# Performance work log

Measured on AMD Instinct MI355X. Metric: run time of the kernel, lower is better.

## Reference

```python
import jax, jax.numpy as jnp
import numpy as np

B, K, D, H, T, S = 8192, 32, 768, 256, 16, 2  # batch, candidates, d_model, hidden, topics, shots
MAX_SHOT = 8
TEMP = 0.1


def _l2n(x, eps=1e-12):
    return x / jnp.clip(jnp.linalg.norm(x, axis=-1, keepdims=True), eps)


def setup_inputs() -> dict:
    key = jax.random.key(0)
    ks = jax.random.split(key, 20)
    f32 = jnp.float32
    rn = lambda k, shape, s: jax.random.normal(k, shape, f32) * s
    inp = {}
    inp['query_emb'] = jax.random.normal(ks[0], (B, D), f32)
    inp['cand_emb'] = jax.random.normal(ks[1], (B, K, D), f32)
    inp['W_in'] = rn(ks[2], (H, D), 0.03)              # input_proj (bias=False)
    inp['Wq_a'] = rn(ks[3], (H, H), 0.05)              # MHA in-proj q
    inp['Wk_a'] = rn(ks[4], (H, H), 0.05)
    inp['Wv_a'] = rn(ks[5], (H, H), 0.05)
    inp['bq_a'] = jnp.zeros((H,), f32)
    inp['bk_a'] = jnp.zeros((H,), f32)
    inp['bv_a'] = jnp.zeros((H,), f32)
    inp['Wo_a'] = rn(ks[6], (H, H), 0.05)              # MHA out-proj
    inp['bo_a'] = jnp.zeros((H,), f32)
    inp['ln_w'] = jnp.ones((H,), f32)
    inp['ln_b'] = jnp.zeros((H,), f32)
    inp['Wq'] = jnp.eye(H, dtype=f32) + rn(ks[7], (H, H), 0.01)   # query_proj (eye init + noise)
    inp['Wc'] = jnp.eye(H, dtype=f32) + rn(ks[8], (H, H), 0.01)   # cand_proj
    inp['W_ih'] = rn(ks[9], (3 * H, H), 0.05)          # GRUCell ih (r,z,n)
    inp['W_hh'] = rn(ks[10], (3 * H, H), 0.05)
    inp['b_ih'] = jnp.zeros((3 * H,), f32)
    inp['b_hh'] = jnp.zeros((3 * H,), f32)
    inp['step_emb'] = rn(ks[11], (MAX_SHOT, H), 0.02)
    inp['topic_protos'] = rn(ks[12], (T, H), 0.02)
    inp['Wqt'] = rn(ks[13], (T, H), 0.05)              # query_topic_head
    inp['bqt'] = jnp.zeros((T,), f32)
    inp['cover_lambda'] = jnp.array(-2.0, f32)
    return inp


def reference(query_emb, cand_emb, W_in, Wq_a, Wk_a, Wv_a, bq_a, bk_a, bv_a,
              Wo_a, bo_a, ln_w, ln_b, Wq, Wc, W_ih, W_hh, b_ih, b_hh,
              step_emb, topic_protos, Wqt, bqt, cover_lambda):
    Bd = query_emb.shape[0]
    # input projection 768 -> 256
    qr = query_emb @ W_in.T                                # [B,H]
    cr = jnp.einsum('bkd,hd->bkh', cand_emb, W_in)         # [B,K,H]
    # single-head cross-attention (query len 1, eval mode -> no dropout)
    q = qr @ Wq_a.T + bq_a
    k = jnp.einsum('bkh,gh->bkg', cr, Wk_a) + bk_a
    v = jnp.einsum('bkh,gh->bkg', cr, Wv_a) + bv_a
    attn = jax.nn.softmax(jnp.einsum('bh,bkh->bk', q, k) / jnp.sqrt(jnp.float32(H)))
    ctx = jnp.einsum('bk,bkh->bh', attn, v) @ Wo_a.T + bo_a
    # residual + LayerNorm
    x = ctx + qr
    mu = jnp.mean(x, -1, keepdims=True)
    var = jnp.var(x, -1, keepdims=True)
    qe = (x - mu) / jnp.sqrt(var + 1e-5) * ln_w + ln_b
    # pointer projections + L2 normalize
    h = _l2n(qe @ Wq.T)                                    # [B,H]
    cn = _l2n(jnp.einsum('bkh,gh->bkg', cr, Wc))           # [B,K,H]
    topic_probs = jax.nn.softmax(jnp.einsum('bkh,th->bkt', cn, _l2n(topic_protos)))  # [B,K,T]
    need = jax.nn.softmax(h @ Wqt.T + bqt)                 # [B,T]
    lam = jax.nn.softplus(cover_lambda)
    sel = jnp.zeros((Bd, K), bool)
    covered = jnp.zeros((Bd, T), jnp.float32)
    rows = jnp.arange(Bd)
    logits, preds = [], []
    for step in range(S):
        h_step = _l2n(h + step_emb[min(step, MAX_SHOT - 1)])
        scores = jnp.einsum('bh,bkh->bk', h_step, cn) / TEMP
        if step > 0:
            uncov = jnp.clip(1.0 - covered, 0.0, 1.0)
            gain = jnp.einsum('bt,bkt->bk', need * uncov, topic_probs)
            scores = scores + lam * gain
        scores = jnp.where(sel, -100.0, scores)
        logits.append(scores)
        idx = jnp.argmax(scores, axis=-1)                  # labels=None -> greedy feedback
        preds.append(idx)
        sel = sel.at[rows, idx].set(True)
        chosen = cn[rows, idx]                             # [B,H]
        covered = jnp.minimum(covered + topic_probs[rows, idx], 1.0)
        # GRUCell update
        gi = chosen @ W_ih.T + b_ih
        gh = h @ W_hh.T + b_hh
        ir, iz, ig = jnp.split(gi, 3, axis=-1)
        hr, hz, hg = jnp.split(gh, 3, axis=-1)
        r = jax.nn.sigmoid(ir + hr)
        z = jax.nn.sigmoid(iz + hz)
        n = jnp.tanh(ig + r * hg)
        h = _l2n((1.0 - z) * n + z * h)
    return jnp.stack(logits, 1), jnp.stack(preds, 1)       # [B,S,K], [B,S]
```

## Files before the change

kernel.cpp:

```cpp
#include <hip/hip_runtime.h>
#include <math.h>

#define B_ 8192
#define K_ 32
#define D_ 768
#define H_ 256
#define T_ 16
#define S_ 2

typedef unsigned int uint;
typedef unsigned short ushort;
typedef __attribute__((ext_vector_type(8))) short bf16x8;
typedef __attribute__((ext_vector_type(4))) float f32x4;

__device__ __forceinline__ float wsum(float v) {
  v += __shfl_xor(v, 32); v += __shfl_xor(v, 16); v += __shfl_xor(v, 8);
  v += __shfl_xor(v, 4);  v += __shfl_xor(v, 2);  v += __shfl_xor(v, 1);
  return v;
}
__device__ __forceinline__ float wmaxr(float v) {
  v = fmaxf(v, __shfl_xor(v, 32)); v = fmaxf(v, __shfl_xor(v, 16));
  v = fmaxf(v, __shfl_xor(v, 8));  v = fmaxf(v, __shfl_xor(v, 4));
  v = fmaxf(v, __shfl_xor(v, 2));  v = fmaxf(v, __shfl_xor(v, 1));
  return v;
}

__device__ __forceinline__ void split4(const float4 f, uint2& h, uint2& lo) {
  const uint ux = __float_as_uint(f.x), uy = __float_as_uint(f.y);
  const uint uz = __float_as_uint(f.z), uw = __float_as_uint(f.w);
  h.x = (uy & 0xFFFF0000u) | (ux >> 16);
  h.y = (uw & 0xFFFF0000u) | (uz >> 16);
  const float rx = f.x - __uint_as_float(ux & 0xFFFF0000u);
  const float ry = f.y - __uint_as_float(uy & 0xFFFF0000u);
  const float rz = f.z - __uint_as_float(uz & 0xFFFF0000u);
  const float rw = f.w - __uint_as_float(uw & 0xFFFF0000u);
  lo.x = (__float_as_uint(ry) & 0xFFFF0000u) | (__float_as_uint(rx) >> 16);
  lo.y = (__float_as_uint(rw) & 0xFFFF0000u) | (__float_as_uint(rz) >> 16);
}


__global__ __launch_bounds__(256)
void fold_kernel(const float* __restrict__ Wk_a, const float* __restrict__ Wv_a,
                 const float* __restrict__ Wc,  const float* __restrict__ W_in,
                 float* __restrict__ WkinT, float* __restrict__ Wv_in,
                 ushort* __restrict__ Bh, ushort* __restrict__ Bl)
{
  const int i = blockIdx.x;
  const int m = blockIdx.y;
  const float* Wx = (m == 0) ? Wk_a : ((m == 1) ? Wv_a : Wc);
  const int t = threadIdx.x;
  float a0 = 0.f, a1 = 0.f, a2 = 0.f;
  for (int k = 0; k < H_; k++) {
    const float wv = Wx[i * H_ + k];
    const float* row = W_in + (size_t)k * D_;
    a0 = fmaf(wv, row[t], a0);
    a1 = fmaf(wv, row[t + 256], a1);
    a2 = fmaf(wv, row[t + 512], a2);
  }
  if (m == 0) {
    WkinT[(size_t)t * H_ + i] = a0;
    WkinT[(size_t)(t + 256) * H_ + i] = a1;
    WkinT[(size_t)(t + 512) * H_ + i] = a2;
  } else if (m == 1) {
    float* o = Wv_in + (size_t)i * D_;
    o[t] = a0; o[t + 256] = a1; o[t + 512] = a2;
  } else {
    const float vals[3] = {a0, a1, a2};
#pragma unroll
    for (int j = 0; j < 3; j++) {
      const int k = t + j * 256;
      const float v = vals[j];
      const int idx = (((k >> 5) * 16 + (i >> 4)) * 64 + ((i & 15) | (((k >> 3) & 3) << 4))) * 8 + (k & 7);
      const uint u = __float_as_uint(v);
      Bh[idx] = (ushort)(u >> 16);
      const float rr = v - __uint_as_float(u & 0xFFFF0000u);
      Bl[idx] = (ushort)(__float_as_uint(rr) >> 16);
    }
  }
}

__global__ __launch_bounds__(256)
void tile_kernel(const float* __restrict__ W, int NB, int K,
                 ushort* __restrict__ Bh, ushort* __restrict__ Bl)
{
  const int n = blockIdx.x, t = threadIdx.x;
  for (int k = t; k < K; k += 256) {
    const float v = W[(size_t)n * K + k];
    const int idx = (((k >> 5) * NB + (n >> 4)) * 64 + ((n & 15) | (((k >> 3) & 3) << 4))) * 8 + (k & 7);
    const uint u = __float_as_uint(v);
    Bh[idx] = (ushort)(u >> 16);
    const float rr = v - __uint_as_float(u & 0xFFFF0000u);
    Bl[idx] = (ushort)(__float_as_uint(rr) >> 16);
  }
}

__global__ __launch_bounds__(256)
void proto_kernel(const float* __restrict__ tpro, float* __restrict__ pro)
{
  const int w = threadIdx.x >> 6, l = threadIdx.x & 63;
  for (int r = w; r < T_; r += 4) {
    const float4 v = *(const float4*)(tpro + (size_t)r * H_ + l * 4);
    const float n = fmaxf(sqrtf(wsum(v.x * v.x + v.y * v.y + v.z * v.z + v.w * v.w)), 1e-12f);
    float4 o; o.x = v.x / n; o.y = v.y / n; o.z = v.z / n; o.w = v.w / n;
    *(float4*)(pro + (size_t)r * H_ + l * 4) = o;
  }
}

__global__ __launch_bounds__(256)
void fold2_kernel(const float* __restrict__ Wq_a, const float* __restrict__ bq_a,
                  const float* __restrict__ bk_a, const float* __restrict__ Wo_a,
                  const float* __restrict__ bo_a, const float* __restrict__ bv_a,
                  const float* __restrict__ Wq,   const float* __restrict__ ln_w,
                  const float* __restrict__ ln_b, const float* __restrict__ WkinT,
                  const float* __restrict__ Wv_in,
                  float* __restrict__ Bqk, float* __restrict__ bqk,
                  float* __restrict__ Wvo, float* __restrict__ bvo,
                  float* __restrict__ Wqp, float* __restrict__ bqp,
                  float* __restrict__ vqbk, float* __restrict__ qcst)
{
  __shared__ float rd_s[4];
  const int n = blockIdx.x, t = threadIdx.x, w = t >> 6, l = t & 63;
  float s = 0.f;
  for (int hh = 0; hh < H_; hh++)
    s = fmaf(Wq_a[hh * H_ + t], WkinT[(size_t)n * H_ + hh], s);
  Bqk[(size_t)n * H_ + t] = s;
  float p = bq_a[t] * WkinT[(size_t)n * H_ + t];
  p = wsum(p);
  if (l == 0) rd_s[w] = p;
  __syncthreads();
  if (t == 0) bqk[n] = rd_s[0] + rd_s[1] + rd_s[2] + rd_s[3];
  if (n < H_) {
    float a0 = 0.f, a1 = 0.f, a2 = 0.f;
    for (int hh = 0; hh < H_; hh++) {
      const float wo = Wo_a[n * H_ + hh];
      const float* rowv = Wv_in + (size_t)hh * D_;
      a0 = fmaf(wo, rowv[t], a0);
      a1 = fmaf(wo, rowv[t + 256], a1);
      a2 = fmaf(wo, rowv[t + 512], a2);
    }
    Wvo[(size_t)n * D_ + t] = a0;
    Wvo[(size_t)n * D_ + t + 256] = a1;
    Wvo[(size_t)n * D_ + t + 512] = a2;
    float pb = Wo_a[n * H_ + t] * bv_a[t];
    pb = wsum(pb);
    __syncthreads();
    if (l == 0) rd_s[w] = pb;
    __syncthreads();
    if (t == 0) bvo[n] = rd_s[0] + rd_s[1] + rd_s[2] + rd_s[3] + bo_a[n];
    Wqp[n * H_ + t] = Wq[n * H_ + t] * ln_w[t];
    float pq = Wq[n * H_ + t] * ln_b[t];
    pq = wsum(pq);
    __syncthreads();
    if (l == 0) rd_s[w] = pq;
    __syncthreads();
    if (t == 0) bqp[n] = rd_s[0] + rd_s[1] + rd_s[2] + rd_s[3];
  }
  if (n == 0) {
    float sv = 0.f;
    for (int hh = 0; hh < H_; hh++) sv = fmaf(bk_a[hh], Wq_a[hh * H_ + t], sv);
    vqbk[t] = sv;
    float pc = bq_a[t] * bk_a[t];
    pc = wsum(pc);
    __syncthreads();
    if (l == 0) rd_s[w] = pc;
    __syncthreads();
    if (t == 0) qcst[0] = rd_s[0] + rd_s[1] + rd_s[2] + rd_s[3];
  }
}

__global__ __launch_bounds__(256)
void gemm_cn(const float* __restrict__ A, const ushort* __restrict__ Bh,
             const ushort* __restrict__ Bl, float* __restrict__ C)
{
  __shared__ __align__(16) ushort AhS[2][2048], AlS[2][2048];
  __shared__ float rsq[64][4];
  const int t = threadIdx.x, l = t & 63, w = t >> 6;
  const int r = t >> 2, kc = t & 3;
  const float* Ag = A + ((size_t)blockIdx.x * 64 + r) * 768 + kc * 8;
  const int aslot = ((r >> 4) * 64 + ((r & 15) | (kc << 4))) * 8;
  const ushort* Bhb = Bh + ((w * 4) * 64 + l) * 8;
  const ushort* Blb = Bl + ((w * 4) * 64 + l) * 8;

  f32x4 acc[4][4];
#pragma unroll
  for (int i = 0; i < 4; i++)
#pragma unroll
    for (int j = 0; j < 4; j++) acc[i][j] = (f32x4)0.f;

  float4 f0 = *(const float4*)(Ag);
  float4 f1 = *(const float4*)(Ag + 4);
  {
    uint2 ha, la, hb, lb;
    split4(f0, ha, la); split4(f1, hb, lb);
    *(uint4*)&AhS[0][aslot] = make_uint4(ha.x, ha.y, hb.x, hb.y);
    *(uint4*)&AlS[0][aslot] = make_uint4(la.x, la.y, lb.x, lb.y);
  }
  f0 = *(const float4*)(Ag + 32);
  f1 = *(const float4*)(Ag + 36);
  __syncthreads();

#pragma unroll 2
  for (int ks = 0; ks < 24; ks++) {
    const int cur = ks & 1;
    uint4 bhv[4], blv[4];
#pragma unroll
    for (int ni = 0; ni < 4; ni++) {
      bhv[ni] = *(const uint4*)(Bhb + ks * 8192 + ni * 512);
      blv[ni] = *(const uint4*)(Blb + ks * 8192 + ni * 512);
    }
    if (ks < 23) {
      uint2 ha, la, hb, lb;
      split4(f0, ha, la); split4(f1, hb, lb);
      *(uint4*)&AhS[cur ^ 1][aslot] = make_uint4(ha.x, ha.y, hb.x, hb.y);
      *(uint4*)&AlS[cur ^ 1][aslot] = make_uint4(la.x, la.y, lb.x, lb.y);
      if (ks < 22) {
        f0 = *(const float4*)(Ag + (ks + 2) * 32);
        f1 = *(const float4*)(Ag + (ks + 2) * 32 + 4);
      }
    }
#pragma unroll
    for (int mi = 0; mi < 4; mi++) {
      const bf16x8 ah = *(const bf16x8*)&AhS[cur][(mi * 64 + l) * 8];
      const bf16x8 al = *(const bf16x8*)&AlS[cur][(mi * 64 + l) * 8];
#pragma unroll
      for (int ni = 0; ni < 4; ni++) {
        const bf16x8 bhf = *(const bf16x8*)&bhv[ni];
        const bf16x8 blf = *(const bf16x8*)&blv[ni];
        acc[mi][ni] = __builtin_amdgcn_mfma_f32_16x16x32_bf16(ah, bhf, acc[mi][ni], 0, 0, 0);
        acc[mi][ni] = __builtin_amdgcn_mfma_f32_16x16x32_bf16(al, bhf, acc[mi][ni], 0, 0, 0);
        acc[mi][ni] = __builtin_amdgcn_mfma_f32_16x16x32_bf16(ah, blf, acc[mi][ni], 0, 0, 0);
      }
    }
    __syncthreads();
  }

#pragma unroll
  for (int mi = 0; mi < 4; mi++)
#pragma unroll
    for (int rg = 0; rg < 4; rg++) {
      float p = 0.f;
#pragma unroll
      for (int ni = 0; ni < 4; ni++) { const float v = acc[mi][ni][rg]; p = fmaf(v, v, p); }
      p += __shfl_xor(p, 1); p += __shfl_xor(p, 2); p += __shfl_xor(p, 4); p += __shfl_xor(p, 8);
      if ((l & 15) == 0) rsq[mi * 16 + (l >> 4) * 4 + rg][w] = p;
    }
  __syncthreads();
  const size_t row0 = (size_t)blockIdx.x * 64;
#pragma unroll
  for (int mi = 0; mi < 4; mi++)
#pragma unroll
    for (int rg = 0; rg < 4; rg++) {
      const int rl = mi * 16 + (l >> 4) * 4 + rg;
      const float ssum = rsq[rl][0] + rsq[rl][1] + rsq[rl][2] + rsq[rl][3];
      const float inv = 1.f / fmaxf(sqrtf(ssum), 1e-12f);
#pragma unroll
      for (int ni = 0; ni < 4; ni++)
        C[(row0 + rl) * H_ + w * 64 + ni * 16 + (l & 15)] = acc[mi][ni][rg] * inv;
    }
}

__global__ __launch_bounds__(256)
void tp_kernel(const float* __restrict__ cn, const float* __restrict__ pro,
               float* __restrict__ tp)
{
  __shared__ float cn_s[16][260];
  __shared__ float pro_s[16][260];
  const int t = threadIdx.x;
  const size_t row0 = (size_t)blockIdx.x * 16;
  const int sr = t >> 4;
#pragma unroll
  for (int j = 0; j < 4; j++) {
    const int c = (t & 15) * 4 + j * 64;
    *(float4*)&cn_s[sr][c] = *(const float4*)(cn + (row0 + sr) * H_ + c);
    *(float4*)&pro_s[sr][c] = *(const float4*)(pro + sr * H_ + c);
  }
  __syncthreads();
  const int r = t >> 4, tt = t & 15;
  float d = 0.f;
#pragma unroll 8
  for (int j = 0; j < 64; j++) {
    const float4 a = *(const float4*)&cn_s[r][j * 4];
    const float4 p = *(const float4*)&pro_s[tt][j * 4];
    d = fmaf(a.x, p.x, d); d = fmaf(a.y, p.y, d);
    d = fmaf(a.z, p.z, d); d = fmaf(a.w, p.w, d);
  }
  float m = d;
  m = fmaxf(m, __shfl_xor(m, 1)); m = fmaxf(m, __shfl_xor(m, 2));
  m = fmaxf(m, __shfl_xor(m, 4)); m = fmaxf(m, __shfl_xor(m, 8));
  const float e = expf(d - m);
  float su = e;
  su += __shfl_xor(su, 1); su += __shfl_xor(su, 2);
  su += __shfl_xor(su, 4); su += __shfl_xor(su, 8);
  tp[(row0 + r) * T_ + tt] = e / su;
}

template<int NKS, int NB, bool BIAS>
__global__ __launch_bounds__(256)
void gemm_bf(const float* __restrict__ A, const ushort* __restrict__ Bh,
             const ushort* __restrict__ Bl, const float* __restrict__ bias,
             float* __restrict__ C)
{
  __shared__ __align__(16) ushort AhS[2][4096], AlS[2][4096];
  const int t = threadIdx.x, l = t & 63, w = t >> 6;
  const int wr = w >> 1, wc = w & 1;
  const int Kd = NKS * 32, N = NB * 16;
  const int r = t >> 1, kc0 = (t & 1) * 2;
  const float* Ag = A + ((size_t)blockIdx.x * 128 + r) * Kd + kc0 * 8;
  const int aslot0 = ((r >> 4) * 64 + ((r & 15) | (kc0 << 4))) * 8;
  const int aslot1 = aslot0 + 128;
  const int nb0 = blockIdx.y * 4 + wc * 2;
  const ushort* Bhb = Bh + (nb0 * 64 + l) * 8;
  const ushort* Blb = Bl + (nb0 * 64 + l) * 8;

  f32x4 acc[4][2];
#pragma unroll
  for (int i = 0; i < 4; i++)
#pragma unroll
    for (int j = 0; j < 2; j++) acc[i][j] = (f32x4)0.f;

  float4 f0 = *(const float4*)(Ag);
  float4 f1 = *(const float4*)(Ag + 4);
  float4 f2 = *(const float4*)(Ag + 8);
  float4 f3 = *(const float4*)(Ag + 12);
  {
    uint2 ha, la, hb, lb;
    split4(f0, ha, la); split4(f1, hb, lb);
    *(uint4*)&AhS[0][aslot0] = make_uint4(ha.x, ha.y, hb.x, hb.y);
    *(uint4*)&AlS[0][aslot0] = make_uint4(la.x, la.y, lb.x, lb.y);
    split4(f2, ha, la); split4(f3, hb, lb);
    *(uint4*)&AhS[0][aslot1] = make_uint4(ha.x, ha.y, hb.x, hb.y);
    *(uint4*)&AlS[0][aslot1] = make_uint4(la.x, la.y, lb.x, lb.y);
  }
  f0 = *(const float4*)(Ag + 32); f1 = *(const float4*)(Ag + 36);
  f2 = *(const float4*)(Ag + 40); f3 = *(const float4*)(Ag + 44);
  __syncthreads();

#pragma unroll 2
  for (int ks = 0; ks < NKS; ks++) {
    const int cur = ks & 1;
    uint4 bhv[2], blv[2];
#pragma unroll
    for (int ni = 0; ni < 2; ni++) {
      bhv[ni] = *(const uint4*)(Bhb + ks * (NB * 512) + ni * 512);
      blv[ni] = *(const uint4*)(Blb + ks * (NB * 512) + ni * 512);
    }
    if (ks < NKS - 1) {
      uint2 ha, la, hb, lb;
      split4(f0, ha, la); split4(f1, hb, lb);
      *(uint4*)&AhS[cur ^ 1][aslot0] = make_uint4(ha.x, ha.y, hb.x, hb.y);
      *(uint4*)&AlS[cur ^ 1][aslot0] = make_uint4(la.x, la.y, lb.x, lb.y);
      split4(f2, ha, la); split4(f3, hb, lb);
      *(uint4*)&AhS[cur ^ 1][aslot1] = make_uint4(ha.x, ha.y, hb.x, hb.y);
      *(uint4*)&AlS[cur ^ 1][aslot1] = make_uint4(la.x, la.y, lb.x, lb.y);
      if (ks < NKS - 2) {
        f0 = *(const float4*)(Ag + (ks + 2) * 32);
        f1 = *(const float4*)(Ag + (ks + 2) * 32 + 4);
        f2 = *(const float4*)(Ag + (ks + 2) * 32 + 8);
        f3 = *(const float4*)(Ag + (ks + 2) * 32 + 12);
      }
    }
#pragma unroll
    for (int mi = 0; mi < 4; mi++) {
      const bf16x8 ah = *(const bf16x8*)&AhS[cur][((wr * 4 + mi) * 64 + l) * 8];
      const bf16x8 al = *(const bf16x8*)&AlS[cur][((wr * 4 + mi) * 64 + l) * 8];
#pragma unroll
      for (int ni = 0; ni < 2; ni++) {
        const bf16x8 bhf = *(const bf16x8*)&bhv[ni];
        const bf16x8 blf = *(const bf16x8*)&blv[ni];
        acc[mi][ni] = __builtin_amdgcn_mfma_f32_16x16x32_bf16(ah, bhf, acc[mi][ni], 0, 0, 0);
        acc[mi][ni] = __builtin_amdgcn_mfma_f32_16x16x32_bf16(al, bhf, acc[mi][ni], 0, 0, 0);
        acc[mi][ni] = __builtin_amdgcn_mfma_f32_16x16x32_bf16(ah, blf, acc[mi][ni], 0, 0, 0);
      }
    }
    __syncthreads();
  }

  const size_t row0 = (size_t)blockIdx.x * 128 + wr * 64;
  const int col0 = blockIdx.y * 64 + wc * 32;
#pragma unroll
  for (int mi = 0; mi < 4; mi++)
#pragma unroll
    for (int ni = 0; ni < 2; ni++) {
      const int col = col0 + ni * 16 + (l & 15);
      const float bb = BIAS ? bias[col] : 0.f;
#pragma unroll
      for (int rg = 0; rg < 4; rg++) {
        const size_t row = row0 + mi * 16 + (l >> 4) * 4 + rg;
        C[row * N + col] = acc[mi][ni][rg] + bb;
      }
    }
}

__global__ __launch_bounds__(256)
void attn_kernel(const float* __restrict__ ce, const float* __restrict__ qkv,
                 const float* __restrict__ qr, const float* __restrict__ vqbk,
                 const float* __restrict__ qcst, float* __restrict__ wce)
{
  __shared__ float4 qk_s[192];
  __shared__ float sc_s[K_];
  __shared__ float at_s[K_];
  __shared__ float rd_s[4];
  const int b = blockIdx.x, t = threadIdx.x;
  const int w = t >> 6, l = t & 63;

  float p = qr[(size_t)b * H_ + t] * vqbk[t];
  p = wsum(p);
  if (l == 0) rd_s[w] = p;
  if (t < 192) qk_s[t] = ((const float4*)qkv)[(size_t)b * 192 + t];
  __syncthreads();
  const float qbk = rd_s[0] + rd_s[1] + rd_s[2] + rd_s[3] + qcst[0];

  const float4* ceb = (const float4*)(ce + (size_t)b * K_ * D_);
#pragma unroll
  for (int cc = 0; cc < 8; cc++) {
    const int c = w * 8 + cc;
    const float4* cr = ceb + c * 192;
    float s = 0.f;
#pragma unroll
    for (int j = 0; j < 3; j++) {
      const float4 f = cr[l + j * 64];
      const float4 q4 = qk_s[l + j * 64];
      s = fmaf(f.x, q4.x, s); s = fmaf(f.y, q4.y, s);
      s = fmaf(f.z, q4.z, s); s = fmaf(f.w, q4.w, s);
    }
    s = wsum(s);
    if (l == 0) sc_s[c] = s + qbk;
  }
  __syncthreads();
  if (w == 0) {
    float s = (l < K_) ? sc_s[l] * (1.f / 16.f) : -1e30f;
    const float m = wmaxr(s);
    float e = (l < K_) ? expf(s - m) : 0.f;
    const float su = wsum(e);
    if (l < K_) at_s[l] = e / su;
  }
  __syncthreads();
  if (t < 192) {
    float4 a = make_float4(0.f, 0.f, 0.f, 0.f);
#pragma unroll
    for (int c = 0; c < K_; c++) {
      const float4 f = ceb[c * 192 + t];
      const float av = at_s[c];
      a.x = fmaf(av, f.x, a.x); a.y = fmaf(av, f.y, a.y);
      a.z = fmaf(av, f.z, a.z); a.w = fmaf(av, f.w, a.w);
    }
    ((float4*)wce)[(size_t)b * 192 + t] = a;
  }
}

__global__ __launch_bounds__(256)
void ln_kernel(const float* __restrict__ xin, const float* __restrict__ res,
               float* __restrict__ xhat)
{
  const int w = threadIdx.x >> 6, l = threadIdx.x & 63;
  const size_t r = (size_t)blockIdx.x * 4 + w;
  const float4 a = *(const float4*)(xin + r * H_ + l * 4);
  const float4 b = *(const float4*)(res + r * H_ + l * 4);
  const float x0 = a.x + b.x, x1 = a.y + b.y, x2 = a.z + b.z, x3 = a.w + b.w;
  const float mu = wsum(x0 + x1 + x2 + x3) * (1.f / H_);
  const float d0 = x0 - mu, d1 = x1 - mu, d2 = x2 - mu, d3 = x3 - mu;
  const float var = wsum(d0 * d0 + d1 * d1 + d2 * d2 + d3 * d3) * (1.f / H_);
  const float isd = 1.f / sqrtf(var + 1e-5f);
  float4 o;
  o.x = d0 * isd; o.y = d1 * isd; o.z = d2 * isd; o.w = d3 * isd;
  *(float4*)(xhat + r * H_ + l * 4) = o;
}

__global__ __launch_bounds__(256)
void h_post(const float* __restrict__ hraw, const float* __restrict__ Wqt,
            const float* __restrict__ bqt, float* __restrict__ h, float* __restrict__ need)
{
  __shared__ float wq_s[T_ * H_];
  for (int i = threadIdx.x; i < T_ * H_; i += 256) wq_s[i] = Wqt[i];
  const int w = threadIdx.x >> 6, l = threadIdx.x & 63;
  const size_t r = (size_t)blockIdx.x * 4 + w;
  const float4 v = *(const float4*)(hraw + r * H_ + l * 4);
  const float n = fmaxf(sqrtf(wsum(v.x * v.x + v.y * v.y + v.z * v.z + v.w * v.w)), 1e-12f);
  float4 hn; hn.x = v.x / n; hn.y = v.y / n; hn.z = v.z / n; hn.w = v.w / n;
  *(float4*)(h + r * H_ + l * 4) = hn;
  __syncthreads();
  float mine = 0.f;
  for (int tt = 0; tt < T_; tt++) {
    const float4 p4 = *(const float4*)(wq_s + tt * H_ + l * 4);
    float p = hn.x * p4.x + hn.y * p4.y + hn.z * p4.z + hn.w * p4.w;
    p = wsum(p);
    if (l == tt) mine = p + bqt[l];
  }
  float s = (l < T_) ? mine : -1e30f;
  const float m = wmaxr(s);
  const float e = (l < T_) ? expf(s - m) : 0.f;
  const float su = wsum(e);
  if (l < T_) need[r * T_ + l] = e / su;
}

template<int STEP>
__global__ __launch_bounds__(256)
void score_kernel(const float* __restrict__ h, const float* __restrict__ se,
                  const float* __restrict__ cn, const float* __restrict__ tp,
                  const float* __restrict__ need, const float* __restrict__ clam,
                  float* __restrict__ covered, int* __restrict__ sel,
                  float* __restrict__ chosen, float* __restrict__ logits,
                  float* __restrict__ preds)
{
  __shared__ __align__(16) float hs_s[H_];
  __shared__ float nu_s[T_];
  __shared__ float sc_s[K_];
  __shared__ float rd_s[4];
  __shared__ int idx_s;
  const int b = blockIdx.x, t = threadIdx.x;
  const int w = t >> 6, l = t & 63;

  const float hv = h[(size_t)b * H_ + t] + se[STEP * H_ + t];
  const float ss = wsum(hv * hv);
  if (l == 0) rd_s[w] = ss;
  if (STEP == 1 && t < T_)
    nu_s[t] = need[(size_t)b * T_ + t] * fminf(fmaxf(1.f - covered[(size_t)b * T_ + t], 0.f), 1.f);
  __syncthreads();
  const float n = fmaxf(sqrtf(rd_s[0] + rd_s[1] + rd_s[2] + rd_s[3]), 1e-12f);
  hs_s[t] = hv / n;
  __syncthreads();

  const float lam = log1pf(expf(clam[0]));
  const float4 hf = *(const float4*)(hs_s + l * 4);
#pragma unroll
  for (int cc = 0; cc < 8; cc++) {
    const int c = w * 8 + cc;
    const float4 cv = *(const float4*)(cn + ((size_t)b * K_ + c) * H_ + l * 4);
    float p = cv.x * hf.x + cv.y * hf.y + cv.z * hf.z + cv.w * hf.w;
    p = wsum(p);
    float s = p / 0.1f;
    if (STEP == 1) {
      float g = (l < T_) ? nu_s[l] * tp[((size_t)b * K_ + c) * T_ + l] : 0.f;
      g = wsum(g);
      s += lam * g;
      if (sel[(size_t)b * K_ + c]) s = -100.f;
    }
    if (l == 0) sc_s[c] = s;
  }
  __syncthreads();
  if (w == 0) {
    float s = (l < K_) ? sc_s[l] : -1e30f;
    int bi = (l < K_) ? l : K_;
#pragma unroll
    for (int o = 32; o; o >>= 1) {
      const float s2 = __shfl_xor(s, o);
      const int i2 = __shfl_xor(bi, o);
      if (s2 > s || (s2 == s && i2 < bi)) { s = s2; bi = i2; }
    }
    if (l == 0) idx_s = bi;
  }
  __syncthreads();
  const int idx = idx_s;
  if (t < K_) logits[(size_t)b * (S_ * K_) + STEP * K_ + t] = sc_s[t];
  if (t == 0) preds[(size_t)b * S_ + STEP] = (float)idx;
  if (STEP == 0) {
    if (t < K_) sel[(size_t)b * K_ + t] = (t == idx) ? 1 : 0;
    if (t < T_) covered[(size_t)b * T_ + t] = fminf(tp[((size_t)b * K_ + idx) * T_ + t], 1.f);
    chosen[(size_t)b * H_ + t] = cn[((size_t)b * K_ + idx) * H_ + t];
  }
}

__global__ __launch_bounds__(256)
void gru_kernel(const float* __restrict__ gi, const float* __restrict__ gh, float* __restrict__ h)
{
  __shared__ float rd_s[4];
  const int b = blockIdx.x, t = threadIdx.x, w = t >> 6, l = t & 63;
  const size_t o = (size_t)b * (3 * H_);
  const float ir = gi[o + t], iz = gi[o + 256 + t], ig = gi[o + 512 + t];
  const float hr = gh[o + t], hz = gh[o + 256 + t], hg = gh[o + 512 + t];
  const float hv = h[(size_t)b * H_ + t];
  const float r = 1.f / (1.f + expf(-(ir + hr)));
  const float z = 1.f / (1.f + expf(-(iz + hz)));
  const float nn = tanhf(ig + r * hg);
  const float x = (1.f - z) * nn + z * hv;
  const float ss = wsum(x * x);
  if (l == 0) rd_s[w] = ss;
  __syncthreads();
  const float n = fmaxf(sqrtf(rd_s[0] + rd_s[1] + rd_s[2] + rd_s[3]), 1e-12f);
  h[(size_t)b * H_ + t] = x / n;
}

extern "C" void kernel_launch(void* const* d_in, const int* in_sizes, int n_in,
                              void* d_out, int out_size, void* d_ws, size_t ws_size,
                              hipStream_t stream)
{
  const float* query_emb = (const float*)d_in[0];
  const float* cand_emb  = (const float*)d_in[1];
  const float* W_in = (const float*)d_in[2];
  const float* Wq_a = (const float*)d_in[3];
  const float* Wk_a = (const float*)d_in[4];
  const float* Wv_a = (const float*)d_in[5];
  const float* bq_a = (const float*)d_in[6];
  const float* bk_a = (const float*)d_in[7];
  const float* bv_a = (const float*)d_in[8];
  const float* Wo_a = (const float*)d_in[9];
  const float* bo_a = (const float*)d_in[10];
  const float* ln_w = (const float*)d_in[11];
  const float* ln_b = (const float*)d_in[12];
  const float* Wq   = (const float*)d_in[13];
  const float* Wc   = (const float*)d_in[14];
  const float* W_ih = (const float*)d_in[15];
  const float* W_hh = (const float*)d_in[16];
  const float* b_ih = (const float*)d_in[17];
  const float* b_hh = (const float*)d_in[18];
  const float* step_emb = (const float*)d_in[19];
  const float* tpro = (const float*)d_in[20];
  const float* Wqt  = (const float*)d_in[21];
  const float* bqt  = (const float*)d_in[22];
  const float* clam = (const float*)d_in[23];

  float* ws = (float*)d_ws;
  size_t o = 0;
  float* WkinT = ws + o; o += (size_t)D_ * H_;
  float* Wv_in = ws + o; o += (size_t)H_ * D_;
  ushort* BhW  = (ushort*)(ws + o); o += 98304;
  ushort* BlW  = (ushort*)(ws + o); o += 98304;
  float* pro   = ws + o; o += (size_t)T_ * H_;
  float* Bqk   = ws + o; o += (size_t)D_ * H_;
  float* bqk   = ws + o; o += 1024;
  float* Wvo   = ws + o; o += (size_t)H_ * D_;
  float* bvo   = ws + o; o += 256;
  float* Wqp   = ws + o; o += (size_t)H_ * H_;
  float* bqp   = ws + o; o += 256;
  float* vqbk  = ws + o; o += 256;
  float* qcst  = ws + o; o += 4;
  ushort* WintH = (ushort*)(ws + o); o += 98304;
  ushort* WintL = (ushort*)(ws + o); o += 98304;
  ushort* BqktH = (ushort*)(ws + o); o += 98304;
  ushort* BqktL = (ushort*)(ws + o); o += 98304;
  ushort* WvotH = (ushort*)(ws + o); o += 98304;
  ushort* WvotL = (ushort*)(ws + o); o += 98304;
  ushort* WqptH = (ushort*)(ws + o); o += 32768;
  ushort* WqptL = (ushort*)(ws + o); o += 32768;
  ushort* WihtH = (ushort*)(ws + o); o += 98304;
  ushort* WihtL = (ushort*)(ws + o); o += 98304;
  ushort* WhhtH = (ushort*)(ws + o); o += 98304;
  ushort* WhhtL = (ushort*)(ws + o); o += 98304;
  float* qr    = ws + o; o += (size_t)B_ * H_;
  float* qkv   = ws + o; o += (size_t)B_ * D_;
  float* wce   = ws + o; o += (size_t)B_ * D_;
  float* ctxb  = ws + o; o += (size_t)B_ * H_;
  float* xhat  = ws + o; o += (size_t)B_ * H_;
  float* h     = ws + o; o += (size_t)B_ * H_;
  float* need  = ws + o; o += (size_t)B_ * T_;
  float* cn    = ws + o; o += (size_t)B_ * K_ * H_;
  float* tp    = ws + o; o += (size_t)B_ * K_ * T_;
  int*   sel   = (int*)(ws + o); o += (size_t)B_ * K_;
  float* cov   = ws + o; o += (size_t)B_ * T_;
  float* chosen= ws + o; o += (size_t)B_ * H_;

  float* out_logits = (float*)d_out;
  float* out_preds  = (float*)d_out + (size_t)B_ * S_ * K_;

  fold_kernel<<<dim3(H_, 3), 256, 0, stream>>>(Wk_a, Wv_a, Wc, W_in, WkinT, Wv_in, BhW, BlW);
  proto_kernel<<<1, 256, 0, stream>>>(tpro, pro);
  fold2_kernel<<<D_, 256, 0, stream>>>(Wq_a, bq_a, bk_a, Wo_a, bo_a, bv_a, Wq, ln_w, ln_b,
                                       WkinT, Wv_in, Bqk, bqk, Wvo, bvo, Wqp, bqp, vqbk, qcst);
  tile_kernel<<<H_, 256, 0, stream>>>(W_in, 16, 768, WintH, WintL);
  tile_kernel<<<D_, 256, 0, stream>>>(Bqk, 48, 256, BqktH, BqktL);
  tile_kernel<<<H_, 256, 0, stream>>>(Wvo, 16, 768, WvotH, WvotL);
  tile_kernel<<<H_, 256, 0, stream>>>(Wqp, 16, 256, WqptH, WqptL);
  tile_kernel<<<D_, 256, 0, stream>>>(W_ih, 48, 256, WihtH, WihtL);
  tile_kernel<<<D_, 256, 0, stream>>>(W_hh, 48, 256, WhhtH, WhhtL);

  gemm_bf<24, 16, false><<<dim3(B_ / 128, 4), 256, 0, stream>>>(query_emb, WintH, WintL, nullptr, qr);
  gemm_bf<8, 48, true><<<dim3(B_ / 128, 12), 256, 0, stream>>>(qr, BqktH, BqktL, bqk, qkv);
  attn_kernel<<<B_, 256, 0, stream>>>(cand_emb, qkv, qr, vqbk, qcst, wce);
  gemm_bf<24, 16, true><<<dim3(B_ / 128, 4), 256, 0, stream>>>(wce, WvotH, WvotL, bvo, ctxb);
  ln_kernel<<<B_ / 4, 256, 0, stream>>>(ctxb, qr, xhat);
  gemm_bf<8, 16, true><<<dim3(B_ / 128, 4), 256, 0, stream>>>(xhat, WqptH, WqptL, bqp, ctxb);
  h_post<<<B_ / 4, 256, 0, stream>>>(ctxb, Wqt, bqt, h, need);

  gemm_cn<<<(B_ * K_) / 64, 256, 0, stream>>>(cand_emb, BhW, BlW, cn);
  tp_kernel<<<(B_ * K_) / 16, 256, 0, stream>>>(cn, pro, tp);

  score_kernel<0><<<B_, 256, 0, stream>>>(h, step_emb, cn, tp, need, clam, cov, sel, chosen, out_logits, out_preds);
  gemm_bf<8, 48, true><<<dim3(B_ / 128, 12), 256, 0, stream>>>(chosen, WihtH, WihtL, b_ih, qkv);
  gemm_bf<8, 48, true><<<dim3(B_ / 128, 12), 256, 0, stream>>>(h, WhhtH, WhhtL, b_hh, wce);
  gru_kernel<<<B_, 256, 0, stream>>>(qkv, wce, h);
  score_kernel<1><<<B_, 256, 0, stream>>>(h, step_emb, cn, tp, need, clam, cov, sel, chosen, out_logits, out_preds);
}
```

Baseline: 1.036 ms.

## Fuse cross-attention into candidate projection GEMM and batch weight tiling launches

The attention-score dot products and the weighted sum over candidate embeddings move into the candidate-projection GEMM, so cand_emb (the largest input) is streamed from DRAM once instead of twice. The six weight-tiling launches are merged into one multi-job kernel. B-fragment loads in both GEMMs are moved next to their MFMA use instead of being prefetched at the top of the k-loop. The fused kernel uses more shared memory and registers and re-reads its candidate tile for the weighted sum, and loading B later may expose global-memory latency.

```diff
diff --git a/kernel.cpp b/kernel.cpp
--- a/kernel.cpp
+++ b/kernel.cpp
@@ -38,6 +38,12 @@
   lo.y = (__float_as_uint(rw) & 0xFFFF0000u) | (__float_as_uint(rz) >> 16);
 }
 
+__device__ __forceinline__ float dot4(const float4 a, const float4 b) {
+  float s = a.x * b.x;
+  s = fmaf(a.y, b.y, s); s = fmaf(a.z, b.z, s); s = fmaf(a.w, b.w, s);
+  return s;
+}
+
 
 __global__ __launch_bounds__(256)
 void fold_kernel(const float* __restrict__ Wk_a, const float* __restrict__ Wv_a,
@@ -79,18 +85,23 @@
   }
 }
 
-__global__ __launch_bounds__(256)
-void tile_kernel(const float* __restrict__ W, int NB, int K,
-                 ushort* __restrict__ Bh, ushort* __restrict__ Bl)
-{
-  const int n = blockIdx.x, t = threadIdx.x;
-  for (int k = t; k < K; k += 256) {
-    const float v = W[(size_t)n * K + k];
-    const int idx = (((k >> 5) * NB + (n >> 4)) * 64 + ((n & 15) | (((k >> 3) & 3) << 4))) * 8 + (k & 7);
+struct TileJob { const float* W; ushort* Bh; ushort* Bl; int NB; int K; int rows; };
+struct TileJobs { TileJob j[6]; };
+
+__global__ __launch_bounds__(256)
+void tile_all(TileJobs jobs)
+{
+  const TileJob J = jobs.j[blockIdx.y];
+  const int n = blockIdx.x;
+  if (n >= J.rows) return;
+  const int t = threadIdx.x;
+  for (int k = t; k < J.K; k += 256) {
+    const float v = J.W[(size_t)n * J.K + k];
+    const int idx = (((k >> 5) * J.NB + (n >> 4)) * 64 + ((n & 15) | (((k >> 3) & 3) << 4))) * 8 + (k & 7);
     const uint u = __float_as_uint(v);
-    Bh[idx] = (ushort)(u >> 16);
+    J.Bh[idx] = (ushort)(u >> 16);
     const float rr = v - __uint_as_float(u & 0xFFFF0000u);
-    Bl[idx] = (ushort)(__float_as_uint(rr) >> 16);
+    J.Bl[idx] = (ushort)(__float_as_uint(rr) >> 16);
   }
 }
 
@@ -169,26 +180,44 @@
 }
 
 __global__ __launch_bounds__(256)
-void gemm_cn(const float* __restrict__ A, const ushort* __restrict__ Bh,
-             const ushort* __restrict__ Bl, float* __restrict__ C)
+void gemm_cn_attn(const float* __restrict__ A, const ushort* __restrict__ Bh,
+                  const ushort* __restrict__ Bl, const float* __restrict__ qkv,
+                  const float* __restrict__ qr, const float* __restrict__ vqbk,
+                  const float* __restrict__ qcst, float* __restrict__ C,
+                  float* __restrict__ wce)
 {
   __shared__ __align__(16) ushort AhS[2][2048], AlS[2][2048];
+  __shared__ __align__(16) float4 qkv_s[384];
+  __shared__ float sc_s[64], at_s[64], qbk_s[2];
   __shared__ float rsq[64][4];
   const int t = threadIdx.x, l = t & 63, w = t >> 6;
   const int r = t >> 2, kc = t & 3;
+  const int tb = t >> 7;
   const float* Ag = A + ((size_t)blockIdx.x * 64 + r) * 768 + kc * 8;
   const int aslot = ((r >> 4) * 64 + ((r & 15) | (kc << 4))) * 8;
   const ushort* Bhb = Bh + ((w * 4) * 64 + l) * 8;
   const ushort* Blb = Bl + ((w * 4) * 64 + l) * 8;
 
+  for (int i = t; i < 384; i += 256)
+    qkv_s[i] = ((const float4*)qkv)[(size_t)blockIdx.x * 384 + i];
+  if (w < 2) {
+    const float4 q4 = ((const float4*)qr)[((size_t)blockIdx.x * 2 + w) * 64 + l];
+    const float4 v4 = ((const float4*)vqbk)[l];
+    float p = wsum(dot4(q4, v4));
+    if (l == 0) qbk_s[w] = p + qcst[0];
+  }
+
   f32x4 acc[4][4];
 #pragma unroll
   for (int i = 0; i < 4; i++)
 #pragma unroll
     for (int j = 0; j < 4; j++) acc[i][j] = (f32x4)0.f;
 
+  float sc = 0.f;
   float4 f0 = *(const float4*)(Ag);
   float4 f1 = *(const float4*)(Ag + 4);
+  __syncthreads();
+  sc += dot4(f0, qkv_s[tb * 192 + kc * 2]) + dot4(f1, qkv_s[tb * 192 + kc * 2 + 1]);
   {
     uint2 ha, la, hb, lb;
     split4(f0, ha, la); split4(f1, hb, lb);
@@ -202,13 +231,9 @@
 #pragma unroll 2
   for (int ks = 0; ks < 24; ks++) {
     const int cur = ks & 1;
-    uint4 bhv[4], blv[4];
-#pragma unroll
-    for (int ni = 0; ni < 4; ni++) {
-      bhv[ni] = *(const uint4*)(Bhb + ks * 8192 + ni * 512);
-      blv[ni] = *(const uint4*)(Blb + ks * 8192 + ni * 512);
-    }
     if (ks < 23) {
+      sc += dot4(f0, qkv_s[tb * 192 + (ks + 1) * 8 + kc * 2]) +
+            dot4(f1, qkv_s[tb * 192 + (ks + 1) * 8 + kc * 2 + 1]);
       uint2 ha, la, hb, lb;
       split4(f0, ha, la); split4(f1, hb, lb);
       *(uint4*)&AhS[cur ^ 1][aslot] = make_uint4(ha.x, ha.y, hb.x, hb.y);
@@ -218,20 +243,55 @@
         f1 = *(const float4*)(Ag + (ks + 2) * 32 + 4);
       }
     }
+    bf16x8 ah[4], al[4];
 #pragma unroll
     for (int mi = 0; mi < 4; mi++) {
-      const bf16x8 ah = *(const bf16x8*)&AhS[cur][(mi * 64 + l) * 8];
-      const bf16x8 al = *(const bf16x8*)&AlS[cur][(mi * 64 + l) * 8];
-#pragma unroll
-      for (int ni = 0; ni < 4; ni++) {
-        const bf16x8 bhf = *(const bf16x8*)&bhv[ni];
-        const bf16x8 blf = *(const bf16x8*)&blv[ni];
-        acc[mi][ni] = __builtin_amdgcn_mfma_f32_16x16x32_bf16(ah, bhf, acc[mi][ni], 0, 0, 0);
-        acc[mi][ni] = __builtin_amdgcn_mfma_f32_16x16x32_bf16(al, bhf, acc[mi][ni], 0, 0, 0);
-        acc[mi][ni] = __builtin_amdgcn_mfma_f32_16x16x32_bf16(ah, blf, acc[mi][ni], 0, 0, 0);
+      ah[mi] = *(const bf16x8*)&AhS[cur][(mi * 64 + l) * 8];
+      al[mi] = *(const bf16x8*)&AlS[cur][(mi * 64 + l) * 8];
+    }
+#pragma unroll
+    for (int ni = 0; ni < 4; ni++) {
+      const bf16x8 bhf = *(const bf16x8*)(Bhb + ks * 8192 + ni * 512);
+      const bf16x8 blf = *(const bf16x8*)(Blb + ks * 8192 + ni * 512);
+#pragma unroll
+      for (int mi = 0; mi < 4; mi++) {
+        acc[mi][ni] = __builtin_amdgcn_mfma_f32_16x16x32_bf16(ah[mi], bhf, acc[mi][ni], 0, 0, 0);
+        acc[mi][ni] = __builtin_amdgcn_mfma_f32_16x16x32_bf16(al[mi], bhf, acc[mi][ni], 0, 0, 0);
+        acc[mi][ni] = __builtin_amdgcn_mfma_f32_16x16x32_bf16(ah[mi], blf, acc[mi][ni], 0, 0, 0);
       }
     }
     __syncthreads();
+  }
+
+  sc += __shfl_xor(sc, 1);
+  sc += __shfl_xor(sc, 2);
+  if ((t & 3) == 0) sc_s[r] = sc;
+  __syncthreads();
+  if (w < 2) {
+    float s = (l < 32) ? (sc_s[w * 32 + l] + qbk_s[w]) * (1.f / 16.f) : -1e30f;
+    const float m = wmaxr(s);
+    const float e = (l < 32) ? expf(s - m) : 0.f;
+    const float su = wsum(e);
+    if (l < 32) at_s[w * 32 + l] = e / su;
+  }
+  __syncthreads();
+#pragma unroll
+  for (int p = 0; p < 2; p++) {
+    const int slot = t + p * 256;
+    if (slot < 384) {
+      const int tb2 = slot >= 192;
+      const int idx = slot - tb2 * 192;
+      const float4* cb = (const float4*)A + ((size_t)blockIdx.x * 64 + tb2 * 32) * 192 + idx;
+      float4 a = make_float4(0.f, 0.f, 0.f, 0.f);
+#pragma unroll 8
+      for (int c = 0; c < 32; c++) {
+        const float av = at_s[tb2 * 32 + c];
+        const float4 f = cb[c * 192];
+        a.x = fmaf(av, f.x, a.x); a.y = fmaf(av, f.y, a.y);
+        a.z = fmaf(av, f.z, a.z); a.w = fmaf(av, f.w, a.w);
+      }
+      ((float4*)wce)[((size_t)blockIdx.x * 2 + tb2) * 192 + idx] = a;
+    }
   }
 
 #pragma unroll
@@ -338,12 +398,6 @@
 #pragma unroll 2
   for (int ks = 0; ks < NKS; ks++) {
     const int cur = ks & 1;
-    uint4 bhv[2], blv[2];
-#pragma unroll
-    for (int ni = 0; ni < 2; ni++) {
-      bhv[ni] = *(const uint4*)(Bhb + ks * (NB * 512) + ni * 512);
-      blv[ni] = *(const uint4*)(Blb + ks * (NB * 512) + ni * 512);
-    }
     if (ks < NKS - 1) {
       uint2 ha, la, hb, lb;
       split4(f0, ha, la); split4(f1, hb, lb);
@@ -365,8 +419,8 @@
       const bf16x8 al = *(const bf16x8*)&AlS[cur][((wr * 4 + mi) * 64 + l) * 8];
 #pragma unroll
       for (int ni = 0; ni < 2; ni++) {
-        const bf16x8 bhf = *(const bf16x8*)&bhv[ni];
-        const bf16x8 blf = *(const bf16x8*)&blv[ni];
+        const bf16x8 bhf = *(const bf16x8*)(Bhb + ks * (NB * 512) + ni * 512);
+        const bf16x8 blf = *(const bf16x8*)(Blb + ks * (NB * 512) + ni * 512);
         acc[mi][ni] = __builtin_amdgcn_mfma_f32_16x16x32_bf16(ah, bhf, acc[mi][ni], 0, 0, 0);
         acc[mi][ni] = __builtin_amdgcn_mfma_f32_16x16x32_bf16(al, bhf, acc[mi][ni], 0, 0, 0);
         acc[mi][ni] = __builtin_amdgcn_mfma_f32_16x16x32_bf16(ah, blf, acc[mi][ni], 0, 0, 0);
@@ -389,63 +443,6 @@
         C[row * N + col] = acc[mi][ni][rg] + bb;
       }
     }
-}
-
-__global__ __launch_bounds__(256)
-void attn_kernel(const float* __restrict__ ce, const float* __restrict__ qkv,
-                 const float* __restrict__ qr, const float* __restrict__ vqbk,
-                 const float* __restrict__ qcst, float* __restrict__ wce)
-{
-  __shared__ float4 qk_s[192];
-  __shared__ float sc_s[K_];
-  __shared__ float at_s[K_];
-  __shared__ float rd_s[4];
-  const int b = blockIdx.x, t = threadIdx.x;
-  const int w = t >> 6, l = t & 63;
-
-  float p = qr[(size_t)b * H_ + t] * vqbk[t];
-  p = wsum(p);
-  if (l == 0) rd_s[w] = p;
-  if (t < 192) qk_s[t] = ((const float4*)qkv)[(size_t)b * 192 + t];
-  __syncthreads();
-  const float qbk = rd_s[0] + rd_s[1] + rd_s[2] + rd_s[3] + qcst[0];
-
-  const float4* ceb = (const float4*)(ce + (size_t)b * K_ * D_);
-#pragma unroll
-  for (int cc = 0; cc < 8; cc++) {
-    const int c = w * 8 + cc;
-    const float4* cr = ceb + c * 192;
-    float s = 0.f;
-#pragma unroll
-    for (int j = 0; j < 3; j++) {
-      const float4 f = cr[l + j * 64];
-      const float4 q4 = qk_s[l + j * 64];
-      s = fmaf(f.x, q4.x, s); s = fmaf(f.y, q4.y, s);
-      s = fmaf(f.z, q4.z, s); s = fmaf(f.w, q4.w, s);
-    }
-    s = wsum(s);
-    if (l == 0) sc_s[c] = s + qbk;
-  }
-  __syncthreads();
-  if (w == 0) {
-    float s = (l < K_) ? sc_s[l] * (1.f / 16.f) : -1e30f;
-    const float m = wmaxr(s);
-    float e = (l < K_) ? expf(s - m) : 0.f;
-    const float su = wsum(e);
-    if (l < K_) at_s[l] = e / su;
-  }
-  __syncthreads();
-  if (t < 192) {
-    float4 a = make_float4(0.f, 0.f, 0.f, 0.f);
-#pragma unroll
-    for (int c = 0; c < K_; c++) {
-      const float4 f = ceb[c * 192 + t];
-      const float av = at_s[c];
-      a.x = fmaf(av, f.x, a.x); a.y = fmaf(av, f.y, a.y);
-      a.z = fmaf(av, f.z, a.z); a.w = fmaf(av, f.w, a.w);
-    }
-    ((float4*)wce)[(size_t)b * 192 + t] = a;
-  }
 }
 
 __global__ __launch_bounds__(256)
@@ -656,22 +653,25 @@
   proto_kernel<<<1, 256, 0, stream>>>(tpro, pro);
   fold2_kernel<<<D_, 256, 0, stream>>>(Wq_a, bq_a, bk_a, Wo_a, bo_a, bv_a, Wq, ln_w, ln_b,
                                        WkinT, Wv_in, Bqk, bqk, Wvo, bvo, Wqp, bqp, vqbk, qcst);
-  tile_kernel<<<H_, 256, 0, stream>>>(W_in, 16, 768, WintH, WintL);
-  tile_kernel<<<D_, 256, 0, stream>>>(Bqk, 48, 256, BqktH, BqktL);
-  tile_kernel<<<H_, 256, 0, stream>>>(Wvo, 16, 768, WvotH, WvotL);
-  tile_kernel<<<H_, 256, 0, stream>>>(Wqp, 16, 256, WqptH, WqptL);
-  tile_kernel<<<D_, 256, 0, stream>>>(W_ih, 48, 256, WihtH, WihtL);
-  tile_kernel<<<D_, 256, 0, stream>>>(W_hh, 48, 256, WhhtH, WhhtL);
+  TileJobs jobs;
+  jobs.j[0] = {W_in, WintH, WintL, 16, 768, 256};
+  jobs.j[1] = {Bqk,  BqktH, BqktL, 48, 256, 768};
+  jobs.j[2] = {Wvo,  WvotH, WvotL, 16, 768, 256};
+  jobs.j[3] = {Wqp,  WqptH, WqptL, 16, 256, 256};
+  jobs.j[4] = {W_ih, WihtH, WihtL, 48, 256, 768};
+  jobs.j[5] = {W_hh, WhhtH, WhhtL, 48, 256, 768};
+  tile_all<<<dim3(768, 6), 256, 0, stream>>>(jobs);
 
   gemm_bf<24, 16, false><<<dim3(B_ / 128, 4), 256, 0, stream>>>(query_emb, WintH, WintL, nullptr, qr);
   gemm_bf<8, 48, true><<<dim3(B_ / 128, 12), 256, 0, stream>>>(qr, BqktH, BqktL, bqk, qkv);
-  attn_kernel<<<B_, 256, 0, stream>>>(cand_emb, qkv, qr, vqbk, qcst, wce);
+
+  gemm_cn_attn<<<(B_ * K_) / 64, 256, 0, stream>>>(cand_emb, BhW, BlW, qkv, qr, vqbk, qcst, cn, wce);
+
   gemm_bf<24, 16, true><<<dim3(B_ / 128, 4), 256, 0, stream>>>(wce, WvotH, WvotL, bvo, ctxb);
   ln_kernel<<<B_ / 4, 256, 0, stream>>>(ctxb, qr, xhat);
   gemm_bf<8, 16, true><<<dim3(B_ / 128, 4), 256, 0, stream>>>(xhat, WqptH, WqptL, bqp, ctxb);
   h_post<<<B_ / 4, 256, 0, stream>>>(ctxb, Wqt, bqt, h, need);
 
-  gemm_cn<<<(B_ * K_) / 64, 256, 0, stream>>>(cand_emb, BhW, BlW, cn);
   tp_kernel<<<(B_ * K_) / 16, 256, 0, stream>>>(cn, pro, tp);
 
   score_kernel<0><<<B_, 256, 0, stream>>>(h, step_emb, cn, tp, need, clam, cov, sel, chosen, out_logits, out_preds);
```

After: 961.1 us. 7.2% less time.
